# Kernel tuning notes

Hardware: AMD Instinct MI355X
Metric: run time of the kernel (lower is better)

## Reference

```python
import jax, jax.numpy as jnp
import numpy as np

# Planck radiance in wavenumber form: B(nu, T) = c1*nu^3 / (exp(c2*nu/T) - 1)
# nu in cm^-1, T in Kelvin, B in W / (m^2 sr cm^-1)
C1 = 1.191042e-8
C2 = 1.4387752
N_TEMPS = 20


def planck_radiance(nu, T):
    return C1 * nu ** 3 / jnp.expm1(C2 * nu / T)


def setup_inputs() -> dict:
    key = jax.random.key(0)
    k1, k2, k3 = jax.random.split(key, 3)
    N, C = 1048576, 54  # 1024x1024 pixels, 54 spectral channels
    wg = jnp.linspace(720.0, 1250.0, C, dtype=jnp.float32)
    v = (wg - wg.min()) / (wg.max() - wg.min())
    pi = 3.14159
    library = jnp.stack([
        jnp.full((C,), 0.98),                      # skin
        0.9 + 0.05 * jnp.sin(2 * pi * v),          # fabric_cotton
        0.15 + 0.1 * v,                            # metal_aluminum
        0.95 - 0.03 * v,                           # vegetation
        0.92 + 0.02 * jnp.sin(4 * pi * v),         # concrete
        0.85 + 0.1 * v,                            # glass
    ]).astype(jnp.float32)
    # realistic LWIR radiance magnitudes (~0.02-0.12 W/m^2/sr/cm^-1)
    s_sky = 0.05 * jax.random.uniform(k1, (C,), dtype=jnp.float32)
    s_ground = 0.08 + 0.02 * jax.random.uniform(k2, (C,), dtype=jnp.float32)
    s_obs = 0.02 + 0.1 * jax.random.uniform(k3, (N, C), dtype=jnp.float32)
    return {"s_obs": s_obs, "s_sky": s_sky, "s_ground": s_ground,
            "library": library, "wavenumber_grid": wg}


def reference(s_obs, s_sky, s_ground, library, wavenumber_grid):
    N, C = s_obs.shape
    M = library.shape[0]
    t_cand = jnp.linspace(250.0, 350.0, N_TEMPS, dtype=s_obs.dtype)
    # All candidate model spectra are pixel-independent (V fixed at 0.5):
    x_amb = 0.5 * s_sky + 0.5 * s_ground                           # [C]
    B = planck_radiance(wavenumber_grid[None, :], t_cand[:, None])  # [T, C]
    s_model = library[:, None, :] * B[None, :, :] \
        + (1.0 - library[:, None, :]) * x_amb                       # [M, T, C]
    cand = s_model.reshape(M * N_TEMPS, C)  # row-major: idx = m*T + t, matches loop order
    # ||s_obs - cand||^2 expanded: memory-bound [N, M*T] loss matrix
    losses = (jnp.sum(s_obs ** 2, axis=-1, keepdims=True)
              - 2.0 * s_obs @ cand.T
              + jnp.sum(cand ** 2, axis=-1))                        # [N, M*T]
    best = jnp.argmin(losses, axis=-1)                              # first-min, matches strict '<'
    best_loss = jnp.take_along_axis(losses, best[:, None], axis=1)[:, 0]
    m_idx = best // N_TEMPS
    t_idx = best % N_TEMPS
    best_t = t_cand[t_idx]                                          # [N]
    best_e = library[m_idx]                                         # [N, C]
    best_v = jnp.full((N,), 0.5, dtype=s_obs.dtype)
    s_recon = best_e * planck_radiance(wavenumber_grid[None, :], best_t[:, None]) \
        + (1.0 - best_e) * x_amb                                    # [N, C]
    texture = best_e.mean(axis=-1)
    beta = jnp.zeros((N, 1), dtype=s_obs.dtype)
    objective = best_loss.mean()
    return (best_t, best_e, best_v, beta, texture, s_recon, objective)
```

## Files before the change

### kernel.cpp

```cpp
#include <hip/hip_runtime.h>
#include <math.h>

#define C_CH 54
#define CP   64
#define NT   20
#define NM   6
#define NK   120
#define BLK  256
#define PPT  2
#define PIX_PER_BLK (BLK * PPT)

typedef float sf16 __attribute__((ext_vector_type(16)));
typedef float sf8  __attribute__((ext_vector_type(8)));

__global__ __launch_bounds__(256) void hadar_prep(
    const float* __restrict__ s_sky, const float* __restrict__ s_ground,
    const float* __restrict__ library, const float* __restrict__ wg,
    float* __restrict__ cand)
{
    __shared__ float xamb[C_CH];
    __shared__ float tc[NT];
    __shared__ float lm[NM];
    const int tid = threadIdx.x;
    if (tid < NT) tc[tid] = 250.0f + (float)tid * (100.0f / 19.0f);
    if (tid < C_CH) xamb[tid] = 0.5f * s_sky[tid] + 0.5f * s_ground[tid];
    if (tid < NM) {
        float s = 0.0f;
        for (int c = 0; c < C_CH; ++c) s += library[tid * C_CH + c];
        lm[tid] = s / (float)C_CH;
    }
    __syncthreads();

    const float c1 = 1.191042e-8f, c2 = 1.4387752f;
    for (int idx = tid; idx < NK * CP; idx += 256) {
        const int k = idx >> 6, c = idx & 63;
        float v = 0.0f;
        if (c < C_CH) {
            const int m = k / NT, t = k - m * NT;
            const float nu = wg[c];
            const float B = c1 * nu * nu * nu / expm1f(c2 * nu / tc[t]);
            const float e = library[m * C_CH + c];
            v = e * B + (1.0f - e) * xamb[c];
        }
        cand[idx] = v;
    }
    __syncthreads();

    if (tid < NK) {
        float s = 0.0f;
        for (int c = 0; c < C_CH; ++c) { float v = cand[tid * CP + c]; s += v * v; }
        const int m = tid / NT, t = tid - m * NT;
        cand[tid * CP + 54] = s;
        cand[tid * CP + 55] = tc[t];
        cand[tid * CP + 56] = lm[m];
    }
}

#define CE(c) ((c) < 16 ? q0[(c)] : (c) < 32 ? q1[(c)-16] : (c) < 48 ? q2[(c)-32] : q3[(c)-48])

__global__ __launch_bounds__(BLK) void hadar_main(
    const float* __restrict__ s_obs,
    const float* __restrict__ library,
    const float* __restrict__ cand,
    float* __restrict__ out, float* __restrict__ partials, int N)
{
    const int tid = threadIdx.x;
    const long long base = (long long)blockIdx.x * PIX_PER_BLK;
    const long long n0 = base + tid;
    const long long n1 = base + BLK + tid;
    const bool v0 = (n0 < N);
    const bool v1 = (n1 < N);

    float row0[C_CH], row1[C_CH];
    if (v0) {
        const float2* rp = (const float2*)(s_obs + n0 * C_CH);
        #pragma unroll
        for (int i = 0; i < C_CH / 2; ++i) {
            float2 w = rp[i];
            row0[2 * i] = w.x; row0[2 * i + 1] = w.y;
        }
    } else {
        #pragma unroll
        for (int c = 0; c < C_CH; ++c) row0[c] = 0.0f;
    }
    if (v1) {
        const float2* rp = (const float2*)(s_obs + n1 * C_CH);
        #pragma unroll
        for (int i = 0; i < C_CH / 2; ++i) {
            float2 w = rp[i];
            row1[2 * i] = w.x; row1[2 * i + 1] = w.y;
        }
    } else {
        #pragma unroll
        for (int c = 0; c < C_CH; ++c) row1[c] = 0.0f;
    }

    float ssq0 = 0.0f, ssq1 = 0.0f;
    #pragma unroll
    for (int c = 0; c < C_CH; ++c) ssq0 += row0[c] * row0[c];
    #pragma unroll
    for (int c = 0; c < C_CH; ++c) ssq1 += row1[c] * row1[c];

    float bl0 = 3.4e38f, bl1 = 3.4e38f;
    int bk0 = NK, bk1 = NK;

    const int wid = __builtin_amdgcn_readfirstlane(tid >> 6);
    const int rot = (int)((blockIdx.x * 4u + (unsigned)wid) % 15u) * 8;

    int kk = rot;
    const float* pk = cand + (size_t)rot * CP;
    #pragma unroll 1
    for (int i = 0; i < NK; ++i) {
        sf16 q0, q1, q2;
        sf8  q3;
        asm volatile("s_load_dwordx16 %0, %1, 0x0"  : "=s"(q0) : "s"(pk));
        asm volatile("s_load_dwordx16 %0, %1, 0x40" : "=s"(q1) : "s"(pk));
        asm volatile("s_load_dwordx16 %0, %1, 0x80" : "=s"(q2) : "s"(pk));
        asm volatile("s_load_dwordx8  %0, %1, 0xc0" : "=s"(q3) : "s"(pk));
        asm volatile("s_waitcnt lgkmcnt(0)" : "+s"(q0), "+s"(q1), "+s"(q2), "+s"(q3));

        float a0[4] = {0.f, 0.f, 0.f, 0.f};
        float a1[4] = {0.f, 0.f, 0.f, 0.f};
        #pragma unroll
        for (int c = 0; c < C_CH; ++c) {
            const float ce = CE(c);
            a0[c & 3] += row0[c] * ce;
            a1[c & 3] += row1[c] * ce;
        }
        const float sq = q3[6];
        const float d0 = (a0[0] + a0[1]) + (a0[2] + a0[3]);
        const float d1 = (a1[0] + a1[1]) + (a1[2] + a1[3]);
        const float l0 = (ssq0 - 2.0f * d0) + sq;
        const float l1 = (ssq1 - 2.0f * d1) + sq;
        if (l0 < bl0 || (l0 == bl0 && kk < bk0)) { bl0 = l0; bk0 = kk; }
        if (l1 < bl1 || (l1 == bl1 && kk < bk1)) { bl1 = l1; bk1 = kk; }

        ++kk; pk += CP;
        if (kk == NK) { kk = 0; pk = cand; }
    }

    if (!v0) bk0 = 0;
    if (!v1) bk1 = 0;

    const size_t NN = (size_t)N;
    const size_t NC = (size_t)C_CH * NN;

    if (v0) {
        const float* cr = cand + (size_t)bk0 * CP;
        out[n0] = cr[55];
        out[NN + NC + n0] = 0.5f;
        out[2 * NN + NC + n0] = 0.0f;
        out[3 * NN + NC + n0] = cr[56];
    }
    if (v1) {
        const float* cr = cand + (size_t)bk1 * CP;
        out[n1] = cr[55];
        out[NN + NC + n1] = 0.5f;
        out[2 * NN + NC + n1] = 0.0f;
        out[3 * NN + NC + n1] = cr[56];
    }

    __shared__ int2 bkm[PIX_PER_BLK];
    bkm[tid]       = make_int2(bk0 * CP, (bk0 / NT) * C_CH);
    bkm[tid + BLK] = make_int2(bk1 * CP, (bk1 / NT) * C_CH);

    float lsum = (v0 ? bl0 : 0.0f) + (v1 ? bl1 : 0.0f);
    __syncthreads();

    {
        float* __restrict__ be = out + NN + (size_t)base * C_CH;
        float* __restrict__ sr = out + 4 * NN + NC + (size_t)base * C_CH;
        int p = tid / C_CH;
        int c = tid - p * C_CH;
        #pragma unroll 4
        for (int j = tid; j < PIX_PER_BLK * C_CH; j += BLK) {
            const int2 o = bkm[p];
            const float ev = library[o.y + c];
            const float sv = cand[o.x + c];
            if (base + p < N) { be[j] = ev; sr[j] = sv; }
            p += 4; c += 40;
            if (c >= C_CH) { c -= C_CH; ++p; }
        }
    }

    __shared__ float red[BLK];
    red[tid] = lsum;
    __syncthreads();
    #pragma unroll
    for (int s = BLK / 2; s > 0; s >>= 1) {
        if (tid < s) red[tid] += red[tid + s];
        __syncthreads();
    }
    if (tid == 0) partials[blockIdx.x] = red[0];
}

__global__ __launch_bounds__(256) void hadar_reduce(
    const float* __restrict__ partials, int nb, float* __restrict__ obj_out, float invN)
{
    __shared__ float red[256];
    float s = 0.0f;
    for (int i = threadIdx.x; i < nb; i += 256) s += partials[i];
    red[threadIdx.x] = s;
    __syncthreads();
    #pragma unroll
    for (int st = 128; st > 0; st >>= 1) {
        if (threadIdx.x < st) red[threadIdx.x] += red[threadIdx.x + st];
        __syncthreads();
    }
    if (threadIdx.x == 0) *obj_out = red[0] * invN;
}

extern "C" void kernel_launch(void* const* d_in, const int* in_sizes, int n_in,
                              void* d_out, int out_size, void* d_ws, size_t ws_size,
                              hipStream_t stream)
{
    const float* s_obs    = (const float*)d_in[0];
    const float* s_sky    = (const float*)d_in[1];
    const float* s_ground = (const float*)d_in[2];
    const float* library  = (const float*)d_in[3];
    const float* wg       = (const float*)d_in[4];
    float* out = (float*)d_out;

    const int N  = in_sizes[0] / C_CH;
    const int nb = (N + PIX_PER_BLK - 1) / PIX_PER_BLK;

    float* ws       = (float*)d_ws;
    float* cand     = ws;
    float* partials = ws + 8192;

    hadar_prep<<<1, 256, 0, stream>>>(s_sky, s_ground, library, wg, cand);
    hadar_main<<<nb, BLK, 0, stream>>>(s_obs, library, cand, out, partials, N);

    const size_t NN = (size_t)N;
    float* obj_out = out + 4 * NN + 2 * (size_t)C_CH * NN;
    hadar_reduce<<<1, 256, 0, stream>>>(partials, nb, obj_out, 1.0f / (float)N);
}
```

Baseline: 777.4 us.

## Stage candidate table in LDS and double-buffer rows in the argmin loop

Copies the 120x64 candidate table into shared memory once per block and reads candidate rows from LDS as float4 vectors into two alternating register buffers. This replaces the per-iteration scalar memory loads and their full lgkmcnt wait, and also drops the per-wave rotation. Gather reads for s_recon now come from LDS too, and occupancy is pinned to two waves per EU. It costs about 30KB of LDS per block, adds vector registers for the buffers, and makes all waves in a CU hit the same LDS addresses.

```diff
diff --git a/kernel.cpp b/kernel.cpp
--- a/kernel.cpp
+++ b/kernel.cpp
@@ -9,9 +9,9 @@
 #define BLK  256
 #define PPT  2
 #define PIX_PER_BLK (BLK * PPT)
-
-typedef float sf16 __attribute__((ext_vector_type(16)));
-typedef float sf8  __attribute__((ext_vector_type(8)));
+#define NF4  (NK * CP / 4)
+
+typedef float f4 __attribute__((ext_vector_type(4)));
 
 __global__ __launch_bounds__(256) void hadar_prep(
     const float* __restrict__ s_sky, const float* __restrict__ s_ground,
@@ -56,14 +56,42 @@
     }
 }
 
-#define CE(c) ((c) < 16 ? q0[(c)] : (c) < 32 ? q1[(c)-16] : (c) < 48 ? q2[(c)-32] : q3[(c)-48])
-
-__global__ __launch_bounds__(BLK) void hadar_main(
+
+#define LOADROW(B, K) { \
+    const f4* __restrict__ Lr = Lc + (size_t)(K) * (CP / 4); \
+    _Pragma("unroll") for (int j = 0; j < 14; ++j) B[j] = Lr[j]; }
+
+#define FMAROW(B, K) { \
+    float a0[4] = {0.f, 0.f, 0.f, 0.f}; \
+    float a1[4] = {0.f, 0.f, 0.f, 0.f}; \
+    _Pragma("unroll") for (int j = 0; j < 14; ++j) { \
+        _Pragma("unroll") for (int e = 0; e < 4; ++e) { \
+            const int c = 4 * j + e; \
+            if (c < C_CH) { \
+                const float ce = B[j][e]; \
+                a0[c & 3] += row0[c] * ce; \
+                a1[c & 3] += row1[c] * ce; \
+            } } } \
+    const float sq = B[13][2]; \
+    const float d0 = (a0[0] + a0[1]) + (a0[2] + a0[3]); \
+    const float d1 = (a1[0] + a1[1]) + (a1[2] + a1[3]); \
+    const float l0 = (ssq0 - 2.0f * d0) + sq; \
+    const float l1 = (ssq1 - 2.0f * d1) + sq; \
+    const bool c0 = l0 < bl0; bl0 = c0 ? l0 : bl0; bk0 = c0 ? (K) : bk0; \
+    const bool c1 = l1 < bl1; bl1 = c1 ? l1 : bl1; bk1 = c1 ? (K) : bk1; }
+
+__global__ __launch_bounds__(BLK)
+__attribute__((amdgpu_waves_per_eu(2, 2)))
+void hadar_main(
     const float* __restrict__ s_obs,
     const float* __restrict__ library,
     const float* __restrict__ cand,
     float* __restrict__ out, float* __restrict__ partials, int N)
 {
+    __shared__ f4 ldsc[NF4];
+    __shared__ int2 bkm[PIX_PER_BLK];
+    __shared__ float red[BLK];
+
     const int tid = threadIdx.x;
     const long long base = (long long)blockIdx.x * PIX_PER_BLK;
     const long long n0 = base + tid;
@@ -71,6 +99,12 @@
     const bool v0 = (n0 < N);
     const bool v1 = (n1 < N);
 
+    {
+        const f4* __restrict__ gc = (const f4*)cand;
+        #pragma unroll
+        for (int j = tid; j < NF4; j += BLK) ldsc[j] = gc[j];
+    }
+
     float row0[C_CH], row1[C_CH];
     if (v0) {
         const float2* rp = (const float2*)(s_obs + n0 * C_CH);
@@ -104,63 +138,43 @@
     float bl0 = 3.4e38f, bl1 = 3.4e38f;
     int bk0 = NK, bk1 = NK;
 
-    const int wid = __builtin_amdgcn_readfirstlane(tid >> 6);
-    const int rot = (int)((blockIdx.x * 4u + (unsigned)wid) % 15u) * 8;
-
-    int kk = rot;
-    const float* pk = cand + (size_t)rot * CP;
+    __syncthreads();
+
+    const f4* __restrict__ Lc = ldsc;
+
+    f4 A[14], B[14];
+    LOADROW(A, 0);
     #pragma unroll 1
-    for (int i = 0; i < NK; ++i) {
-        sf16 q0, q1, q2;
-        sf8  q3;
-        asm volatile("s_load_dwordx16 %0, %1, 0x0"  : "=s"(q0) : "s"(pk));
-        asm volatile("s_load_dwordx16 %0, %1, 0x40" : "=s"(q1) : "s"(pk));
-        asm volatile("s_load_dwordx16 %0, %1, 0x80" : "=s"(q2) : "s"(pk));
-        asm volatile("s_load_dwordx8  %0, %1, 0xc0" : "=s"(q3) : "s"(pk));
-        asm volatile("s_waitcnt lgkmcnt(0)" : "+s"(q0), "+s"(q1), "+s"(q2), "+s"(q3));
-
-        float a0[4] = {0.f, 0.f, 0.f, 0.f};
-        float a1[4] = {0.f, 0.f, 0.f, 0.f};
-        #pragma unroll
-        for (int c = 0; c < C_CH; ++c) {
-            const float ce = CE(c);
-            a0[c & 3] += row0[c] * ce;
-            a1[c & 3] += row1[c] * ce;
-        }
-        const float sq = q3[6];
-        const float d0 = (a0[0] + a0[1]) + (a0[2] + a0[3]);
-        const float d1 = (a1[0] + a1[1]) + (a1[2] + a1[3]);
-        const float l0 = (ssq0 - 2.0f * d0) + sq;
-        const float l1 = (ssq1 - 2.0f * d1) + sq;
-        if (l0 < bl0 || (l0 == bl0 && kk < bk0)) { bl0 = l0; bk0 = kk; }
-        if (l1 < bl1 || (l1 == bl1 && kk < bk1)) { bl1 = l1; bk1 = kk; }
-
-        ++kk; pk += CP;
-        if (kk == NK) { kk = 0; pk = cand; }
-    }
+    for (int k = 0; k < NK - 2; k += 2) {
+        LOADROW(B, k + 1);
+        FMAROW(A, k);
+        LOADROW(A, k + 2);
+        FMAROW(B, k + 1);
+    }
+    LOADROW(B, NK - 1);
+    FMAROW(A, NK - 2);
+    FMAROW(B, NK - 1);
 
     if (!v0) bk0 = 0;
     if (!v1) bk1 = 0;
 
     const size_t NN = (size_t)N;
     const size_t NC = (size_t)C_CH * NN;
+    const float* __restrict__ Lf = (const float*)ldsc;
 
     if (v0) {
-        const float* cr = cand + (size_t)bk0 * CP;
-        out[n0] = cr[55];
+        out[n0] = Lf[bk0 * CP + 55];
         out[NN + NC + n0] = 0.5f;
         out[2 * NN + NC + n0] = 0.0f;
-        out[3 * NN + NC + n0] = cr[56];
+        out[3 * NN + NC + n0] = Lf[bk0 * CP + 56];
     }
     if (v1) {
-        const float* cr = cand + (size_t)bk1 * CP;
-        out[n1] = cr[55];
+        out[n1] = Lf[bk1 * CP + 55];
         out[NN + NC + n1] = 0.5f;
         out[2 * NN + NC + n1] = 0.0f;
-        out[3 * NN + NC + n1] = cr[56];
-    }
-
-    __shared__ int2 bkm[PIX_PER_BLK];
+        out[3 * NN + NC + n1] = Lf[bk1 * CP + 56];
+    }
+
     bkm[tid]       = make_int2(bk0 * CP, (bk0 / NT) * C_CH);
     bkm[tid + BLK] = make_int2(bk1 * CP, (bk1 / NT) * C_CH);
 
@@ -176,14 +190,13 @@
         for (int j = tid; j < PIX_PER_BLK * C_CH; j += BLK) {
             const int2 o = bkm[p];
             const float ev = library[o.y + c];
-            const float sv = cand[o.x + c];
+            const float sv = Lf[o.x + c];
             if (base + p < N) { be[j] = ev; sr[j] = sv; }
             p += 4; c += 40;
             if (c >= C_CH) { c -= C_CH; ++p; }
         }
     }
 
-    __shared__ float red[BLK];
     red[tid] = lsum;
     __syncthreads();
     #pragma unroll
```

Measured after the change: 1.383 ms. 1.78x slower.
